# Performance work log

Measured on AMD Instinct MI355X. Metric: run time of the kernel, lower is better.

Reference implementation:

```python
import jax, jax.numpy as jnp
import numpy as np

DIM = 2048
N_HEADS = 16
N_KV_HEADS = 4
HEAD_DIM = DIM // N_HEADS  # 128
N_REP = N_HEADS // N_KV_HEADS
EPS = 1e-6


def rmsnorm(x, w):
    norm = jax.lax.rsqrt(jnp.mean(x * x, axis=-1, keepdims=True) + EPS)
    return x * norm * w


def apply_rope(xq, xk, freqs_cis):
    # xq: (B,S,Hq,D), xk: (B,S,Hk,D); freqs_cis: (S, D/2, 2) -> (cos, sin)
    cos = freqs_cis[None, :, None, :, 0]  # (1,S,1,D/2)
    sin = freqs_cis[None, :, None, :, 1]

    def rot(x):
        xr = x.reshape(*x.shape[:-1], HEAD_DIM // 2, 2)
        x0, x1 = xr[..., 0], xr[..., 1]
        o0 = x0 * cos - x1 * sin
        o1 = x0 * sin + x1 * cos
        return jnp.stack([o0, o1], axis=-1).reshape(x.shape)

    return rot(xq), rot(xk)


def setup_inputs() -> dict:
    key = jax.random.key(0)
    k1, k2, k3, k4, k5, k6 = jax.random.split(key, 6)
    B, S = 2, 2048
    x = jax.random.normal(k1, (B, S, DIM), dtype=jnp.float32)
    x_mask = jnp.ones((B, S), dtype=bool)
    freqs_cis = jax.random.uniform(k2, (S, HEAD_DIM // 2, 2), dtype=jnp.float32)
    qkv_out = (N_HEADS + 2 * N_KV_HEADS) * HEAD_DIM  # 3072
    w_qkv = jax.random.normal(k3, (qkv_out, DIM), dtype=jnp.float32) * (DIM ** -0.5)
    w_out = jax.random.normal(k4, (DIM, N_HEADS * HEAD_DIM), dtype=jnp.float32) * (DIM ** -0.5)
    qn_w = jnp.ones((HEAD_DIM,), dtype=jnp.float32)
    kn_w = jnp.ones((HEAD_DIM,), dtype=jnp.float32)
    return {"x": x, "x_mask": x_mask, "freqs_cis": freqs_cis,
            "w_qkv": w_qkv, "w_out": w_out, "qn_w": qn_w, "kn_w": kn_w}


def reference(x, x_mask, freqs_cis, w_qkv, w_out, qn_w, kn_w):
    B, S, _ = x.shape
    qkv = x @ w_qkv.T  # (B,S,3072)
    dq = N_HEADS * HEAD_DIM
    dkv = N_KV_HEADS * HEAD_DIM
    xq = qkv[..., :dq].reshape(B, S, N_HEADS, HEAD_DIM)
    xk = qkv[..., dq:dq + dkv].reshape(B, S, N_KV_HEADS, HEAD_DIM)
    xv = qkv[..., dq + dkv:].reshape(B, S, N_KV_HEADS, HEAD_DIM)
    xq = rmsnorm(xq, qn_w)
    xk = rmsnorm(xk, kn_w)
    xq, xk = apply_rope(xq, xk, freqs_cis)
    # GQA: repeat kv heads
    xk = jnp.repeat(xk, N_REP, axis=2)  # (B,S,H,D)
    xv = jnp.repeat(xv, N_REP, axis=2)
    # SDPA: (B,H,S,D)
    q = jnp.moveaxis(xq, 1, 2)
    k = jnp.moveaxis(xk, 1, 2)
    v = jnp.moveaxis(xv, 1, 2)
    scale = HEAD_DIM ** -0.5
    scores = jnp.einsum('bhqd,bhkd->bhqk', q, k) * scale
    bias = jnp.where(x_mask[:, None, None, :], 0.0, -jnp.inf).astype(q.dtype)
    attn = jax.nn.softmax(scores + bias, axis=-1)
    out = jnp.einsum('bhqk,bhkd->bhqd', attn, v)
    out = jnp.moveaxis(out, 1, 2).reshape(B, S, N_HEADS * HEAD_DIM)
    return out @ w_out.T
```

## Files before the change

### kernel.cpp

```cpp
#include <hip/hip_runtime.h>
#include <hip/hip_bf16.h>

#define DIMSZ 2048
#define SLEN  2048
#define NH    16
#define NKV   4
#define HD    128
#define NTOK  4096
#define QKVN  3072

typedef __bf16 bf16x8 __attribute__((ext_vector_type(8)));
typedef __bf16 bf16x4 __attribute__((ext_vector_type(4)));
typedef short  s16x4  __attribute__((ext_vector_type(4)));
typedef float  floatx4 __attribute__((ext_vector_type(4)));

__device__ __forceinline__ void async16(const __bf16* g, __bf16* l) {
    __builtin_amdgcn_global_load_lds(
        (const __attribute__((address_space(1))) void*)g,
        (__attribute__((address_space(3))) void*)l, 16, 0, 0);
}

__device__ __forceinline__ floatx4 mfma16x16x16_bf16(s16x4 a, s16x4 b, floatx4 c) {
#if __has_builtin(__builtin_amdgcn_mfma_f32_16x16x16bf16_1k)
    return __builtin_amdgcn_mfma_f32_16x16x16bf16_1k(a, b, c, 0, 0, 0);
#else
    asm volatile("v_mfma_f32_16x16x16_bf16 %0, %1, %2, %0"
                 : "+v"(c) : "v"(a), "v"(b));
    return c;
#endif
}

__global__ __launch_bounds__(256) void cvt_f32_bf16(const float* __restrict__ src,
                                                    __bf16* __restrict__ dst, int n) {
    int i = (blockIdx.x * 256 + threadIdx.x) * 8;
    if (i >= n) return;
    float4 a = *(const float4*)(src + i);
    float4 b = *(const float4*)(src + i + 4);
    bf16x8 o;
    o[0] = (__bf16)a.x; o[1] = (__bf16)a.y; o[2] = (__bf16)a.z; o[3] = (__bf16)a.w;
    o[4] = (__bf16)b.x; o[5] = (__bf16)b.y; o[6] = (__bf16)b.z; o[7] = (__bf16)b.w;
    *(bf16x8*)(dst + i) = o;
}

template <typename CT>
__global__ __launch_bounds__(256) void gemm_bt(const __bf16* __restrict__ A,
                                               const __bf16* __restrict__ B,
                                               CT* __restrict__ C,
                                               int M, int N, int K) {
    __shared__ __align__(16) __bf16 As[128 * 64];
    __shared__ __align__(16) __bf16 Bs[128 * 64];
    const int tid  = threadIdx.x;
    const int wave = tid >> 6, lane = tid & 63;
    const int lr = lane & 15, lq = lane >> 4;
    const int wm = (wave >> 1) * 64, wn = (wave & 1) * 64;
    const int tm0 = blockIdx.y * 128, tn0 = blockIdx.x * 128;

    floatx4 acc[4][4] = {};

    for (int k0 = 0; k0 < K; k0 += 64) {
#pragma unroll
        for (int i = 0; i < 4; ++i) {
            int c   = tid + 256 * i;
            int row = c >> 3, col = (c & 7) * 8;
            async16(&A[(size_t)(tm0 + row) * K + k0 + col], &As[c * 8]);
            async16(&B[(size_t)(tn0 + row) * K + k0 + col], &Bs[c * 8]);
        }
        __syncthreads();
#pragma unroll
        for (int kk = 0; kk < 2; ++kk) {
            bf16x8 af[4], bg[4];
#pragma unroll
            for (int i = 0; i < 4; ++i)
                af[i] = *(const bf16x8*)&As[(wm + i * 16 + lr) * 64 + kk * 32 + lq * 8];
#pragma unroll
            for (int j = 0; j < 4; ++j)
                bg[j] = *(const bf16x8*)&Bs[(wn + j * 16 + lr) * 64 + kk * 32 + lq * 8];
#pragma unroll
            for (int i = 0; i < 4; ++i)
#pragma unroll
                for (int j = 0; j < 4; ++j)
                    acc[i][j] = __builtin_amdgcn_mfma_f32_16x16x32_bf16(
                        af[i], bg[j], acc[i][j], 0, 0, 0);
        }
        __syncthreads();
    }
#pragma unroll
    for (int i = 0; i < 4; ++i)
#pragma unroll
        for (int j = 0; j < 4; ++j)
#pragma unroll
            for (int r = 0; r < 4; ++r) {
                int row = tm0 + wm + i * 16 + lq * 4 + r;
                int col = tn0 + wn + j * 16 + lr;
                C[(size_t)row * N + col] = (CT)acc[i][j][r];
            }
}

__global__ __launch_bounds__(64) void norm_rope(const __bf16* __restrict__ qkv,
                                                const float* __restrict__ freqs,
                                                const float* __restrict__ qn_w,
                                                const float* __restrict__ kn_w,
                                                __bf16* __restrict__ Qo,
                                                __bf16* __restrict__ Ko) {
    const int tok = blockIdx.x;
    const int hd  = blockIdx.y;
    const int t   = threadIdx.x;
    const int s   = tok & (SLEN - 1);
    const int b   = tok >> 11;
    const bool isq = hd < NH;
    const int h    = isq ? hd : hd - NH;
    const int base = isq ? h * HD : (NH * HD + h * HD);

    const __bf16* src = qkv + (size_t)tok * QKVN + base + 2 * t;
    float x0 = (float)src[0], x1 = (float)src[1];
    float ss = x0 * x0 + x1 * x1;
#pragma unroll
    for (int off = 32; off >= 1; off >>= 1) ss += __shfl_xor(ss, off);
    float rs = rsqrtf(ss * (1.0f / 128.0f) + 1e-6f);

    const float* w = isq ? qn_w : kn_w;
    float w0 = w[2 * t], w1 = w[2 * t + 1];
    float cs = freqs[(s * 64 + t) * 2 + 0];
    float sn = freqs[(s * 64 + t) * 2 + 1];
    float n0 = x0 * rs * w0, n1 = x1 * rs * w1;
    float o0 = n0 * cs - n1 * sn;
    float o1 = n0 * sn + n1 * cs;
    if (isq) { o0 *= 0.08838834764831845f; o1 *= 0.08838834764831845f; }

    __bf16* dst = isq ? (Qo + (((size_t)(b * NH + h)) * SLEN + s) * HD + 2 * t)
                      : (Ko + (((size_t)(b * NKV + h)) * SLEN + s) * HD + 2 * t);
    dst[0] = (__bf16)o0;
    dst[1] = (__bf16)o1;
}

__global__ __launch_bounds__(256) void v_transpose(const __bf16* __restrict__ qkv,
                                                   __bf16* __restrict__ VT) {
    __shared__ __align__(16) __bf16 L[64 * 136];
    const int st  = blockIdx.x;
    const int kh  = blockIdx.y;
    const int b   = blockIdx.z;
    const int tid = threadIdx.x;
#pragma unroll
    for (int i = 0; i < 4; ++i) {
        int c = tid + 256 * i;
        int srow = c >> 4, dc = (c & 15) * 8;
        int tok = b * SLEN + st * 64 + srow;
        *(int4*)&L[srow * 136 + dc] =
            *(const int4*)&qkv[(size_t)tok * QKVN + 2560 + kh * HD + dc];
    }
    __syncthreads();
#pragma unroll
    for (int i = 0; i < 4; ++i) {
        int c = tid + 256 * i;
        int d = c >> 3, sc = (c & 7) * 8;
        __bf16 tmp[8];
#pragma unroll
        for (int j = 0; j < 8; ++j) tmp[j] = L[(sc + j) * 136 + d];
        *(int4*)&VT[(((size_t)(b * NKV + kh)) * HD + d) * SLEN + st * 64 + sc] =
            *(int4*)tmp;
    }
}

__global__ __launch_bounds__(256) void attn(const __bf16* __restrict__ Q,
                                            const __bf16* __restrict__ Kn,
                                            const __bf16* __restrict__ VT,
                                            __bf16* __restrict__ O) {
    __shared__ __align__(16) __bf16 Ks[64 * 136];
    __shared__ __align__(16) __bf16 Vts[128 * 72];
    const int qt  = blockIdx.x;
    const int h   = blockIdx.y;
    const int b   = blockIdx.z;
    const int tid = threadIdx.x;
    const int w = tid >> 6, lane = tid & 63, lr = lane & 15, lq = lane >> 4;
    const int kh = h >> 2;

    const __bf16* Qb = Q  + ((size_t)(b * NH + h))   * SLEN * HD;
    const __bf16* Kb = Kn + ((size_t)(b * NKV + kh)) * SLEN * HD;
    const __bf16* Vb = VT + ((size_t)(b * NKV + kh)) * HD * SLEN;

    bf16x8 qf[4];
    const int q0 = qt * 64 + w * 16 + lr;
#pragma unroll
    for (int kc = 0; kc < 4; ++kc)
        qf[kc] = *(const bf16x8*)&Qb[(size_t)q0 * HD + kc * 32 + lq * 8];

    floatx4 oacc[8] = {};
    float m_i = -1e30f, l_i = 0.f;

    for (int kt = 0; kt < 32; ++kt) {
#pragma unroll
        for (int i = 0; i < 4; ++i) {
            int c = tid + 256 * i;
            int krow = c >> 4, dc = (c & 15) * 8;
            *(int4*)&Ks[krow * 136 + dc] =
                *(const int4*)&Kb[(size_t)(kt * 64 + krow) * HD + dc];
            int d = c >> 3, sc = (c & 7) * 8;
            *(int4*)&Vts[d * 72 + sc] =
                *(const int4*)&Vb[(size_t)d * SLEN + kt * 64 + sc];
        }
        __syncthreads();

        floatx4 sacc[4] = {};
#pragma unroll
        for (int nt = 0; nt < 4; ++nt)
#pragma unroll
            for (int kc = 0; kc < 4; ++kc) {
                bf16x8 kf = *(const bf16x8*)&Ks[(nt * 16 + lr) * 136 + kc * 32 + lq * 8];
                sacc[nt] = __builtin_amdgcn_mfma_f32_16x16x32_bf16(kf, qf[kc], sacc[nt], 0, 0, 0);
            }

        float tm = -1e30f;
#pragma unroll
        for (int nt = 0; nt < 4; ++nt)
            tm = fmaxf(tm, fmaxf(fmaxf(sacc[nt][0], sacc[nt][1]),
                                 fmaxf(sacc[nt][2], sacc[nt][3])));
        tm = fmaxf(tm, __shfl_xor(tm, 16));
        tm = fmaxf(tm, __shfl_xor(tm, 32));
        float mnew = fmaxf(m_i, tm);
        float rsum = 0.f;
        s16x4 pf[4];
#pragma unroll
        for (int nt = 0; nt < 4; ++nt) {
            bf16x4 pb;
#pragma unroll
            for (int r = 0; r < 4; ++r) {
                float p = __expf(sacc[nt][r] - mnew);
                rsum += p;
                pb[r] = (__bf16)p;
            }
            pf[nt] = *(s16x4*)&pb;
        }
        rsum += __shfl_xor(rsum, 16);
        rsum += __shfl_xor(rsum, 32);
        float alpha = __expf(m_i - mnew);
        l_i = l_i * alpha + rsum;
        m_i = mnew;
#pragma unroll
        for (int dt = 0; dt < 8; ++dt)
#pragma unroll
            for (int r = 0; r < 4; ++r) oacc[dt][r] *= alpha;

#pragma unroll
        for (int dt = 0; dt < 8; ++dt)
#pragma unroll
            for (int nt = 0; nt < 4; ++nt) {
                s16x4 vf = *(const s16x4*)&Vts[(dt * 16 + lr) * 72 + nt * 16 + lq * 4];
                oacc[dt] = mfma16x16x16_bf16(vf, pf[nt], oacc[dt]);
            }
        __syncthreads();
    }

    float inv = 1.0f / l_i;
    __bf16* orow = O + (((size_t)(b * SLEN + q0)) * NH + h) * HD;
#pragma unroll
    for (int dt = 0; dt < 8; ++dt) {
        bf16x4 ob;
#pragma unroll
        for (int r = 0; r < 4; ++r) ob[r] = (__bf16)(oacc[dt][r] * inv);
        *(bf16x4*)&orow[dt * 16 + lq * 4] = ob;
    }
}

extern "C" void kernel_launch(void* const* d_in, const int* in_sizes, int n_in,
                              void* d_out, int out_size, void* d_ws, size_t ws_size,
                              hipStream_t stream) {
    const float* x     = (const float*)d_in[0];
    const float* freqs = (const float*)d_in[2];
    const float* w_qkv = (const float*)d_in[3];
    const float* w_out = (const float*)d_in[4];
    const float* qn_w  = (const float*)d_in[5];
    const float* kn_w  = (const float*)d_in[6];
    float* out = (float*)d_out;

    char* ws = (char*)d_ws;
    __bf16* qkv = (__bf16*)ws;
    __bf16* Qb  = (__bf16*)(ws + 25165824ull);
    __bf16* Kb  = (__bf16*)(ws + 25165824ull + 16777216);
    __bf16* VTb = (__bf16*)(ws + 25165824ull + 16777216 + 4194304);
    __bf16* xb  = (__bf16*)(ws + 50331648ull);
    __bf16* wqb = (__bf16*)(ws + 50331648ull + 16777216);
    __bf16* wob = (__bf16*)(ws + 50331648ull + 16777216 + 12582912);
    __bf16* Ob  = (__bf16*)ws;

    cvt_f32_bf16<<<NTOK * DIMSZ / 2048, 256, 0, stream>>>(x, xb, NTOK * DIMSZ);
    cvt_f32_bf16<<<QKVN * DIMSZ / 2048, 256, 0, stream>>>(w_qkv, wqb, QKVN * DIMSZ);
    cvt_f32_bf16<<<DIMSZ * DIMSZ / 2048, 256, 0, stream>>>(w_out, wob, DIMSZ * DIMSZ);
    gemm_bt<__bf16><<<dim3(QKVN / 128, NTOK / 128), 256, 0, stream>>>(
        xb, wqb, qkv, NTOK, QKVN, DIMSZ);
    norm_rope<<<dim3(NTOK, NH + NKV), 64, 0, stream>>>(qkv, freqs, qn_w, kn_w, Qb, Kb);
    v_transpose<<<dim3(32, NKV, 2), 256, 0, stream>>>(qkv, VTb);
    attn<<<dim3(32, NH, 2), 256, 0, stream>>>(Qb, Kb, VTb, Ob);
    gemm_bt<float><<<dim3(DIMSZ / 128, NTOK / 128), 256, 0, stream>>>(
        Ob, wob, out, NTOK, DIMSZ, DIMSZ);
}
```

Baseline: 423.0 us.

## Double-buffer attention K/V with async swizzled LDS loads and two query groups per wave

The attention kernel now stages K and V tiles with asynchronous global-to-LDS loads into two buffers, using an XOR swizzle instead of padding. The next tile loads while the current one is computed, and one barrier per iteration is removed. Each wave now handles 32 queries, so every K/V fragment read from LDS feeds two MFMAs, and the grid is halved. The online-softmax running max and rescaling are dropped, which relies on scores staying bounded after the RMS norm and risks overflow with large norm weights. norm_rope also packs four tokens per 256-thread block.

```diff
diff --git a/kernel.cpp b/kernel.cpp
--- a/kernel.cpp
+++ b/kernel.cpp
@@ -96,15 +96,15 @@
             }
 }
 
-__global__ __launch_bounds__(64) void norm_rope(const __bf16* __restrict__ qkv,
-                                                const float* __restrict__ freqs,
-                                                const float* __restrict__ qn_w,
-                                                const float* __restrict__ kn_w,
-                                                __bf16* __restrict__ Qo,
-                                                __bf16* __restrict__ Ko) {
-    const int tok = blockIdx.x;
+__global__ __launch_bounds__(256) void norm_rope(const __bf16* __restrict__ qkv,
+                                                 const float* __restrict__ freqs,
+                                                 const float* __restrict__ qn_w,
+                                                 const float* __restrict__ kn_w,
+                                                 __bf16* __restrict__ Qo,
+                                                 __bf16* __restrict__ Ko) {
+    const int tok = blockIdx.x * 4 + (threadIdx.x >> 6);
     const int hd  = blockIdx.y;
-    const int t   = threadIdx.x;
+    const int t   = threadIdx.x & 63;
     const int s   = tok & (SLEN - 1);
     const int b   = tok >> 11;
     const bool isq = hd < NH;
@@ -165,8 +165,8 @@
                                             const __bf16* __restrict__ Kn,
                                             const __bf16* __restrict__ VT,
                                             __bf16* __restrict__ O) {
-    __shared__ __align__(16) __bf16 Ks[64 * 136];
-    __shared__ __align__(16) __bf16 Vts[128 * 72];
+    __shared__ __align__(16) __bf16 Ks [2][64 * 128];
+    __shared__ __align__(16) __bf16 Vts[2][128 * 64];
     const int qt  = blockIdx.x;
     const int h   = blockIdx.y;
     const int b   = blockIdx.z;
@@ -178,86 +178,99 @@
     const __bf16* Kb = Kn + ((size_t)(b * NKV + kh)) * SLEN * HD;
     const __bf16* Vb = VT + ((size_t)(b * NKV + kh)) * HD * SLEN;
 
-    bf16x8 qf[4];
-    const int q0 = qt * 64 + w * 16 + lr;
-#pragma unroll
-    for (int kc = 0; kc < 4; ++kc)
-        qf[kc] = *(const bf16x8*)&Qb[(size_t)q0 * HD + kc * 32 + lq * 8];
-
-    floatx4 oacc[8] = {};
-    float m_i = -1e30f, l_i = 0.f;
-
-    for (int kt = 0; kt < 32; ++kt) {
+    bf16x8 qf[2][4];
+    const int qbase = qt * 128 + w * 32;
+#pragma unroll
+    for (int g2 = 0; g2 < 2; ++g2)
+#pragma unroll
+        for (int kc = 0; kc < 4; ++kc)
+            qf[g2][kc] = *(const bf16x8*)
+                &Qb[(size_t)(qbase + g2 * 16 + lr) * HD + kc * 32 + lq * 8];
+
+    floatx4 oacc[2][8] = {};
+    float l_i[2] = {0.f, 0.f};
+
+    auto stage = [&](int buf, int kt) {
 #pragma unroll
         for (int i = 0; i < 4; ++i) {
             int c = tid + 256 * i;
-            int krow = c >> 4, dc = (c & 15) * 8;
-            *(int4*)&Ks[krow * 136 + dc] =
-                *(const int4*)&Kb[(size_t)(kt * 64 + krow) * HD + dc];
-            int d = c >> 3, sc = (c & 7) * 8;
-            *(int4*)&Vts[d * 72 + sc] =
-                *(const int4*)&Vb[(size_t)d * SLEN + kt * 64 + sc];
-        }
+            int row = c >> 4, u = c & 15;
+            int g = u ^ (row & 7);
+            async16(&Kb[(size_t)(kt * 64 + row) * HD + g * 8], &Ks[buf][c * 8]);
+        }
+#pragma unroll
+        for (int i = 0; i < 4; ++i) {
+            int c = tid + 256 * i;
+            int d = c >> 3, u = c & 7;
+            int g = u ^ (d & 7);
+            async16(&Vb[(size_t)d * SLEN + kt * 64 + g * 8], &Vts[buf][c * 8]);
+        }
+    };
+
+    stage(0, 0);
+    for (int kt = 0; kt < 32; ++kt) {
+        const int buf = kt & 1;
         __syncthreads();
-
-        floatx4 sacc[4] = {};
+        if (kt < 31) stage(buf ^ 1, kt + 1);
+
+        floatx4 sacc[2][4] = {};
 #pragma unroll
         for (int nt = 0; nt < 4; ++nt)
 #pragma unroll
             for (int kc = 0; kc < 4; ++kc) {
-                bf16x8 kf = *(const bf16x8*)&Ks[(nt * 16 + lr) * 136 + kc * 32 + lq * 8];
-                sacc[nt] = __builtin_amdgcn_mfma_f32_16x16x32_bf16(kf, qf[kc], sacc[nt], 0, 0, 0);
+                bf16x8 kf = *(const bf16x8*)
+                    &Ks[buf][(nt * 16 + lr) * 128 + ((kc * 4 + lq) ^ (lr & 7)) * 8];
+                sacc[0][nt] = __builtin_amdgcn_mfma_f32_16x16x32_bf16(
+                    kf, qf[0][kc], sacc[0][nt], 0, 0, 0);
+                sacc[1][nt] = __builtin_amdgcn_mfma_f32_16x16x32_bf16(
+                    kf, qf[1][kc], sacc[1][nt], 0, 0, 0);
             }
 
-        float tm = -1e30f;
-#pragma unroll
-        for (int nt = 0; nt < 4; ++nt)
-            tm = fmaxf(tm, fmaxf(fmaxf(sacc[nt][0], sacc[nt][1]),
-                                 fmaxf(sacc[nt][2], sacc[nt][3])));
-        tm = fmaxf(tm, __shfl_xor(tm, 16));
-        tm = fmaxf(tm, __shfl_xor(tm, 32));
-        float mnew = fmaxf(m_i, tm);
-        float rsum = 0.f;
-        s16x4 pf[4];
-#pragma unroll
-        for (int nt = 0; nt < 4; ++nt) {
-            bf16x4 pb;
-#pragma unroll
-            for (int r = 0; r < 4; ++r) {
-                float p = __expf(sacc[nt][r] - mnew);
-                rsum += p;
-                pb[r] = (__bf16)p;
+        s16x4 pf[2][4];
+#pragma unroll
+        for (int g2 = 0; g2 < 2; ++g2) {
+            float rsum = 0.f;
+#pragma unroll
+            for (int nt = 0; nt < 4; ++nt) {
+                bf16x4 pb;
+#pragma unroll
+                for (int r = 0; r < 4; ++r) {
+                    float p = __expf(sacc[g2][nt][r]);
+                    rsum += p;
+                    pb[r] = (__bf16)p;
+                }
+                pf[g2][nt] = *(s16x4*)&pb;
             }
-            pf[nt] = *(s16x4*)&pb;
-        }
-        rsum += __shfl_xor(rsum, 16);
-        rsum += __shfl_xor(rsum, 32);
-        float alpha = __expf(m_i - mnew);
-        l_i = l_i * alpha + rsum;
-        m_i = mnew;
+            l_i[g2] += rsum;
+        }
+
 #pragma unroll
         for (int dt = 0; dt < 8; ++dt)
 #pragma unroll
-            for (int r = 0; r < 4; ++r) oacc[dt][r] *= alpha;
-
-#pragma unroll
-        for (int dt = 0; dt < 8; ++dt)
-#pragma unroll
             for (int nt = 0; nt < 4; ++nt) {
-                s16x4 vf = *(const s16x4*)&Vts[(dt * 16 + lr) * 72 + nt * 16 + lq * 4];
-                oacc[dt] = mfma16x16x16_bf16(vf, pf[nt], oacc[dt]);
+                int u = (2 * nt + (lq >> 1)) ^ (lr & 7);
+                s16x4 vf = *(const s16x4*)
+                    &Vts[buf][(dt * 16 + lr) * 64 + u * 8 + (lq & 1) * 4];
+                oacc[0][dt] = mfma16x16x16_bf16(vf, pf[0][nt], oacc[0][dt]);
+                oacc[1][dt] = mfma16x16x16_bf16(vf, pf[1][nt], oacc[1][dt]);
             }
-        __syncthreads();
-    }
-
-    float inv = 1.0f / l_i;
-    __bf16* orow = O + (((size_t)(b * SLEN + q0)) * NH + h) * HD;
-#pragma unroll
-    for (int dt = 0; dt < 8; ++dt) {
-        bf16x4 ob;
-#pragma unroll
-        for (int r = 0; r < 4; ++r) ob[r] = (__bf16)(oacc[dt][r] * inv);
-        *(bf16x4*)&orow[dt * 16 + lq * 4] = ob;
+    }
+
+#pragma unroll
+    for (int g2 = 0; g2 < 2; ++g2) {
+        float l = l_i[g2];
+        l += __shfl_xor(l, 16);
+        l += __shfl_xor(l, 32);
+        float inv = 1.0f / l;
+        int qs = qbase + g2 * 16 + lr;
+        __bf16* orow = O + (((size_t)(b * SLEN + qs)) * NH + h) * HD;
+#pragma unroll
+        for (int dt = 0; dt < 8; ++dt) {
+            bf16x4 ob;
+#pragma unroll
+            for (int r = 0; r < 4; ++r) ob[r] = (__bf16)(oacc[g2][dt][r] * inv);
+            *(bf16x4*)&orow[dt * 16 + lq * 4] = ob;
+        }
     }
 }
 
@@ -285,11 +298,15 @@
     cvt_f32_bf16<<<NTOK * DIMSZ / 2048, 256, 0, stream>>>(x, xb, NTOK * DIMSZ);
     cvt_f32_bf16<<<QKVN * DIMSZ / 2048, 256, 0, stream>>>(w_qkv, wqb, QKVN * DIMSZ);
     cvt_f32_bf16<<<DIMSZ * DIMSZ / 2048, 256, 0, stream>>>(w_out, wob, DIMSZ * DIMSZ);
+
     gemm_bt<__bf16><<<dim3(QKVN / 128, NTOK / 128), 256, 0, stream>>>(
         xb, wqb, qkv, NTOK, QKVN, DIMSZ);
-    norm_rope<<<dim3(NTOK, NH + NKV), 64, 0, stream>>>(qkv, freqs, qn_w, kn_w, Qb, Kb);
+
+    norm_rope<<<dim3(NTOK / 4, NH + NKV), 256, 0, stream>>>(qkv, freqs, qn_w, kn_w, Qb, Kb);
     v_transpose<<<dim3(32, NKV, 2), 256, 0, stream>>>(qkv, VTb);
-    attn<<<dim3(32, NH, 2), 256, 0, stream>>>(Qb, Kb, VTb, Ob);
+
+    attn<<<dim3(SLEN / 128, NH, 2), 256, 0, stream>>>(Qb, Kb, VTb, Ob);
+
     gemm_bt<float><<<dim3(DIMSZ / 128, NTOK / 128), 256, 0, stream>>>(
         Ob, wob, out, NTOK, DIMSZ, DIMSZ);
 }
```

New measurement: 369.4 us. 12.7% less time.
